# Kernel tuning notes

Hardware: AMD Instinct MI355X
Metric: run time of the kernel (lower is better)

Reference implementation:

```python
import jax, jax.numpy as jnp
import numpy as np

B = 8192
N_IN = 16 * 12 * 64  # 12288
H0, H1, H2 = 256, 32, 32
OUTPUT_SCALE = 300.0
WDL_SCALE = 200.0


def setup_inputs() -> dict:
    key = jax.random.key(0)
    ks = jax.random.split(key, 12)
    # In real NNUE these are ~30-hot binary vectors; math is identical for dense rand.
    white_features = (jax.random.uniform(ks[0], (B, N_IN)) < 0.0025).astype(jnp.float32)
    black_features = (jax.random.uniform(ks[1], (B, N_IN)) < 0.0025).astype(jnp.float32)
    side = jax.random.randint(ks[2], (B,), 0, 2).astype(bool)
    ft_std = np.sqrt(2.0 / (22 + H1))
    ft_w = jax.random.normal(ks[3], (H0, N_IN)) * ft_std
    ft_b = jnp.zeros((H0,))
    def xavier(k, fan_out, fan_in):
        std = np.sqrt(2.0 / (fan_in + fan_out))
        return jax.random.normal(k, (fan_out, fan_in)) * std
    l1_w = xavier(ks[4], H1, 2 * H0)
    l1_b = jnp.zeros((H1,))
    l2_w = xavier(ks[5], H2, H1)
    l2_b = jnp.zeros((H2,))
    l3_w = xavier(ks[6], 1, H2)
    l3_b = jnp.zeros((1,))
    return {"white_features": white_features, "black_features": black_features,
            "side": side, "ft_w": ft_w, "ft_b": ft_b, "l1_w": l1_w, "l1_b": l1_b,
            "l2_w": l2_w, "l2_b": l2_b, "l3_w": l3_w, "l3_b": l3_b}


def reference(white_features, black_features, side, ft_w, ft_b,
              l1_w, l1_b, l2_w, l2_b, l3_w, l3_b):
    w = white_features @ ft_w.T + ft_b  # [B, H0]
    b = black_features @ ft_w.T + ft_b  # [B, H0]
    s = side[:, None]  # [B, 1] bool
    # side-to-move first: white -> [w, b], black -> [b, w]
    acc = jnp.where(s, jnp.concatenate([w, b], axis=1),
                    jnp.concatenate([b, w], axis=1))  # [B, 2*H0]
    o0 = jnp.clip(acc, 0.0, 1.0)
    o1 = jnp.clip(o0 @ l1_w.T + l1_b, 0.0, 1.0)
    o2 = jnp.clip(o1 @ l2_w.T + l2_b, 0.0, 1.0)
    o3 = (o2 @ l3_w.T + l3_b) * OUTPUT_SCALE  # [B, 1]
    return jax.nn.sigmoid(o3 / WDL_SCALE)
```

## Files before the change

### kernel.cpp

```cpp
#include <hip/hip_runtime.h>
#include <math.h>


#define NIN   12288
#define NF4   3072
#define FPT   12
#define H0    256
#define MAXF  192

__device__ __forceinline__ unsigned char mask4(uint4 u) {
    return (unsigned char)((u.x ? 1u : 0u) | (u.y ? 2u : 0u) |
                           (u.z ? 4u : 0u) | (u.w ? 8u : 0u));
}
__device__ __forceinline__ float bflo(unsigned u) { return __uint_as_float(u << 16); }
__device__ __forceinline__ float bfhi(unsigned u) { return __uint_as_float(u & 0xFFFF0000u); }

__global__ __launch_bounds__(256) void transpose_ftw_bf16(const float* __restrict__ src,
                                                          unsigned short* __restrict__ dst) {
    __shared__ float tile[32][33];
    const int jb = blockIdx.x * 32;
    const int hb = blockIdx.y * 32;
    const int tx = threadIdx.x;
    const int ty = threadIdx.y;
#pragma unroll
    for (int r = 0; r < 32; r += 8)
        tile[ty + r][tx] = src[(size_t)(hb + ty + r) * NIN + jb + tx];
    __syncthreads();
#pragma unroll
    for (int r = 0; r < 32; r += 8) {
        const unsigned u = __float_as_uint(tile[tx][ty + r]);
        const unsigned short h = (unsigned short)((u + 0x7FFFu + ((u >> 16) & 1u)) >> 16);
        dst[(size_t)(jb + ty + r) * H0 + hb + tx] = h;
    }
}

__global__ __launch_bounds__(256, 4) void scan_kernel(const uint4* __restrict__ white,
                                                      const uint4* __restrict__ black,
                                                      unsigned char* __restrict__ wbm,
                                                      unsigned char* __restrict__ bbm,
                                                      int total)
{
    const int i0 = blockIdx.x * 2048 + threadIdx.x;
    if (i0 + 7 * 256 < total) {
        uint4 w[8], b[8];
#pragma unroll
        for (int k = 0; k < 8; ++k) w[k] = white[i0 + k * 256];
#pragma unroll
        for (int k = 0; k < 8; ++k) b[k] = black[i0 + k * 256];
#pragma unroll
        for (int k = 0; k < 8; ++k) wbm[i0 + k * 256] = mask4(w[k]);
#pragma unroll
        for (int k = 0; k < 8; ++k) bbm[i0 + k * 256] = mask4(b[k]);
    } else {
#pragma unroll
        for (int k = 0; k < 8; ++k) {
            const int i = i0 + k * 256;
            if (i < total) { wbm[i] = mask4(white[i]); bbm[i] = mask4(black[i]); }
        }
    }
}

__global__ __launch_bounds__(256) void gather_kernel(
    const int* __restrict__ side,
    const unsigned* __restrict__ tab,
    const float* __restrict__ ft_b,
    const float* __restrict__ l1_w,
    const float* __restrict__ l1_b,
    const float* __restrict__ l2_w,
    const float* __restrict__ l2_b,
    const float* __restrict__ l3_w,
    const float* __restrict__ l3_b,
    const unsigned char* __restrict__ wbm,
    const unsigned char* __restrict__ bbm,
    float* __restrict__ out)
{
    __shared__ int w_list[MAXF];
    __shared__ int b_list[MAXF];
    __shared__ int w_cnt, b_cnt;
    __shared__ float sh_o0[512] __attribute__((aligned(16)));
    __shared__ float sh_o1[32];
    __shared__ float sh_o2[32];

    const int s   = blockIdx.x;
    const int tid = threadIdx.x;

    if (tid == 0) { w_cnt = 0; b_cnt = 0; }
    __syncthreads();

    const unsigned* wrow = (const unsigned*)(wbm + (size_t)s * NF4);
    const unsigned* brow = (const unsigned*)(bbm + (size_t)s * NF4);
#pragma unroll
    for (int q = 0; q < 3; ++q) {
        const int d = q * 256 + tid;
        unsigned v = wrow[d];
        while (v) {
            const int bpos = __ffs(v) - 1;
            const int j = ((d * 4 + (bpos >> 3)) << 2) + (bpos & 7);
            const int p = atomicAdd(&w_cnt, 1);
            if (p < MAXF) w_list[p] = j;
            v &= v - 1;
        }
        unsigned vb = brow[d];
        while (vb) {
            const int bpos = __ffs(vb) - 1;
            const int j = ((d * 4 + (bpos >> 3)) << 2) + (bpos & 7);
            const int p = atomicAdd(&b_cnt, 1);
            if (p < MAXF) b_list[p] = j;
            vb &= vb - 1;
        }
    }
    __syncthreads();

    const int wn = min(w_cnt, MAXF);
    const int bn = min(b_cnt, MAXF);

    const int  h       = tid & 127;
    const bool isWhite = (tid < 128);
    const int* lst     = isWhite ? w_list : b_list;
    const int  n       = isWhite ? wn : bn;
    const unsigned* colp = tab + h;

    float accx = ft_b[2 * h];
    float accy = ft_b[2 * h + 1];
    {
        int k = 0;
        for (; k + 8 <= n; k += 8) {
            const unsigned u0 = colp[(size_t)lst[k]     * 128];
            const unsigned u1 = colp[(size_t)lst[k + 1] * 128];
            const unsigned u2 = colp[(size_t)lst[k + 2] * 128];
            const unsigned u3 = colp[(size_t)lst[k + 3] * 128];
            const unsigned u4 = colp[(size_t)lst[k + 4] * 128];
            const unsigned u5 = colp[(size_t)lst[k + 5] * 128];
            const unsigned u6 = colp[(size_t)lst[k + 6] * 128];
            const unsigned u7 = colp[(size_t)lst[k + 7] * 128];
            accx += ((bflo(u0) + bflo(u1)) + (bflo(u2) + bflo(u3))) +
                    ((bflo(u4) + bflo(u5)) + (bflo(u6) + bflo(u7)));
            accy += ((bfhi(u0) + bfhi(u1)) + (bfhi(u2) + bfhi(u3))) +
                    ((bfhi(u4) + bfhi(u5)) + (bfhi(u6) + bfhi(u7)));
        }
        for (; k < n; ++k) {
            const unsigned u = colp[(size_t)lst[k] * 128];
            accx += bflo(u);
            accy += bfhi(u);
        }
    }
    const float cx = fminf(fmaxf(accx, 0.f), 1.f);
    const float cy = fminf(fmaxf(accy, 0.f), 1.f);
    const bool sd = (side[s] != 0);
    const int base = (isWhite == sd) ? 0 : 256;
    sh_o0[base + 2 * h]     = cx;
    sh_o0[base + 2 * h + 1] = cy;
    __syncthreads();

    {
        const int o = tid >> 3;
        const int p = tid & 7;
        const float4* wp = (const float4*)(l1_w + (o * 512 + p * 64));
        const float4* xp = (const float4*)(sh_o0 + p * 64);
        float sum = 0.f;
#pragma unroll
        for (int i = 0; i < 16; ++i) {
            const int v = (2 * p + i) & 15;
            float4 w4 = wp[v];
            float4 x4 = xp[v];
            sum += w4.x * x4.x + w4.y * x4.y + w4.z * x4.z + w4.w * x4.w;
        }
        sum += __shfl_down(sum, 4, 8);
        sum += __shfl_down(sum, 2, 8);
        sum += __shfl_down(sum, 1, 8);
        if (p == 0) sh_o1[o] = fminf(fmaxf(sum + l1_b[o], 0.f), 1.f);
    }
    __syncthreads();

    if (tid < 32) {
        float sum = 0.f;
#pragma unroll
        for (int k = 0; k < 32; ++k) sum += l2_w[tid * 32 + k] * sh_o1[k];
        sh_o2[tid] = fminf(fmaxf(sum + l2_b[tid], 0.f), 1.f);
    }
    __syncthreads();

    if (tid < 32) {
        float p = l3_w[tid] * sh_o2[tid];
        p += __shfl_down(p, 16, 32);
        p += __shfl_down(p, 8, 32);
        p += __shfl_down(p, 4, 32);
        p += __shfl_down(p, 2, 32);
        p += __shfl_down(p, 1, 32);
        if (tid == 0) {
            const float o3 = (p + l3_b[0]) * 300.0f;
            out[s] = 1.0f / (1.0f + expf(-o3 / 200.0f));
        }
    }
}

__global__ __launch_bounds__(256) void nnue_kernel(
    const float* __restrict__ white, const float* __restrict__ black,
    const int* __restrict__ side, const float* __restrict__ ftw,
    const float* __restrict__ ft_b, const float* __restrict__ l1_w,
    const float* __restrict__ l1_b, const float* __restrict__ l2_w,
    const float* __restrict__ l2_b, const float* __restrict__ l3_w,
    const float* __restrict__ l3_b, float* __restrict__ out)
{
    __shared__ int w_list[MAXF];
    __shared__ int b_list[MAXF];
    __shared__ int w_cnt, b_cnt;
    __shared__ float sh_o0[512] __attribute__((aligned(16)));
    __shared__ float sh_o1[32];
    __shared__ float sh_o2[32];
    const int s = blockIdx.x, tid = threadIdx.x;
    if (tid == 0) { w_cnt = 0; b_cnt = 0; }
    __syncthreads();
    const uint4* wrow = (const uint4*)(white + (size_t)s * NIN);
    const uint4* brow = (const uint4*)(black + (size_t)s * NIN);
#pragma unroll
    for (int i = 0; i < FPT; ++i) {
        const int v = i * 256 + tid;
        uint4 u = wrow[v];
        if (u.x | u.y | u.z | u.w) {
            if (u.x) { int p = atomicAdd(&w_cnt, 1); if (p < MAXF) w_list[p] = v * 4 + 0; }
            if (u.y) { int p = atomicAdd(&w_cnt, 1); if (p < MAXF) w_list[p] = v * 4 + 1; }
            if (u.z) { int p = atomicAdd(&w_cnt, 1); if (p < MAXF) w_list[p] = v * 4 + 2; }
            if (u.w) { int p = atomicAdd(&w_cnt, 1); if (p < MAXF) w_list[p] = v * 4 + 3; }
        }
        uint4 b = brow[v];
        if (b.x | b.y | b.z | b.w) {
            if (b.x) { int p = atomicAdd(&b_cnt, 1); if (p < MAXF) b_list[p] = v * 4 + 0; }
            if (b.y) { int p = atomicAdd(&b_cnt, 1); if (p < MAXF) b_list[p] = v * 4 + 1; }
            if (b.z) { int p = atomicAdd(&b_cnt, 1); if (p < MAXF) b_list[p] = v * 4 + 2; }
            if (b.w) { int p = atomicAdd(&b_cnt, 1); if (p < MAXF) b_list[p] = v * 4 + 3; }
        }
    }
    __syncthreads();
    const int wn = min(w_cnt, MAXF), bn = min(b_cnt, MAXF);
    const float bias = ft_b[tid];
    float wacc = bias, bacc = bias;
    for (int k = 0; k < wn; ++k) wacc += ftw[(size_t)tid * NIN + w_list[k]];
    for (int k = 0; k < bn; ++k) bacc += ftw[(size_t)tid * NIN + b_list[k]];
    const float ow = fminf(fmaxf(wacc, 0.f), 1.f);
    const float ob = fminf(fmaxf(bacc, 0.f), 1.f);
    const bool sd = (side[s] != 0);
    sh_o0[tid] = sd ? ow : ob;
    sh_o0[256 + tid] = sd ? ob : ow;
    __syncthreads();
    {
        const int o = tid >> 3, p = tid & 7;
        const float4* wp = (const float4*)(l1_w + (o * 512 + p * 64));
        const float4* xp = (const float4*)(sh_o0 + p * 64);
        float sum = 0.f;
#pragma unroll
        for (int i = 0; i < 16; ++i) {
            const int v = (2 * p + i) & 15;
            float4 w4 = wp[v]; float4 x4 = xp[v];
            sum += w4.x * x4.x + w4.y * x4.y + w4.z * x4.z + w4.w * x4.w;
        }
        sum += __shfl_down(sum, 4, 8);
        sum += __shfl_down(sum, 2, 8);
        sum += __shfl_down(sum, 1, 8);
        if (p == 0) sh_o1[o] = fminf(fmaxf(sum + l1_b[o], 0.f), 1.f);
    }
    __syncthreads();
    if (tid < 32) {
        float sum = 0.f;
#pragma unroll
        for (int k = 0; k < 32; ++k) sum += l2_w[tid * 32 + k] * sh_o1[k];
        sh_o2[tid] = fminf(fmaxf(sum + l2_b[tid], 0.f), 1.f);
    }
    __syncthreads();
    if (tid < 32) {
        float p = l3_w[tid] * sh_o2[tid];
        p += __shfl_down(p, 16, 32);
        p += __shfl_down(p, 8, 32);
        p += __shfl_down(p, 4, 32);
        p += __shfl_down(p, 2, 32);
        p += __shfl_down(p, 1, 32);
        if (tid == 0) {
            const float o3 = (p + l3_b[0]) * 300.0f;
            out[s] = 1.0f / (1.0f + expf(-o3 / 200.0f));
        }
    }
}

extern "C" void kernel_launch(void* const* d_in, const int* in_sizes, int n_in,
                              void* d_out, int out_size, void* d_ws, size_t ws_size,
                              hipStream_t stream) {
    const float* white = (const float*)d_in[0];
    const float* black = (const float*)d_in[1];
    const int*   side  = (const int*)d_in[2];
    const float* ft_w  = (const float*)d_in[3];
    const float* ft_b  = (const float*)d_in[4];
    const float* l1_w  = (const float*)d_in[5];
    const float* l1_b  = (const float*)d_in[6];
    const float* l2_w  = (const float*)d_in[7];
    const float* l2_b  = (const float*)d_in[8];
    const float* l3_w  = (const float*)d_in[9];
    const float* l3_b  = (const float*)d_in[10];
    float*       out   = (float*)d_out;

    const int B = in_sizes[2];
    const size_t t_bytes  = (size_t)NIN * H0 * 2;
    const size_t bm_bytes = (size_t)B * NF4;
    const size_t need     = t_bytes + 2 * bm_bytes;

    if (ws_size >= need) {
        unsigned short* ftw_t = (unsigned short*)d_ws;
        unsigned char*  wbm   = (unsigned char*)d_ws + t_bytes;
        unsigned char*  bbm   = wbm + bm_bytes;
        const int total = B * NF4;

        hipLaunchKernelGGL(transpose_ftw_bf16, dim3(NIN / 32, H0 / 32), dim3(32, 8), 0, stream,
                           ft_w, ftw_t);
        hipLaunchKernelGGL(scan_kernel, dim3((total + 2047) / 2048), dim3(256), 0, stream,
                           (const uint4*)white, (const uint4*)black, wbm, bbm, total);
        hipLaunchKernelGGL(gather_kernel, dim3(B), dim3(256), 0, stream,
                           side, (const unsigned*)ftw_t, ft_b, l1_w, l1_b, l2_w, l2_b,
                           l3_w, l3_b, wbm, bbm, out);
    } else {
        hipLaunchKernelGGL(nnue_kernel, dim3(B), dim3(256), 0, stream,
                           white, black, side, ft_w, ft_b, l1_w, l1_b, l2_w, l2_b,
                           l3_w, l3_b, out);
    }
}
```

Measured before the change: 883.8 us.

## Fuse dense feature scan into gather kernel, dropping bitmask intermediate pass

Removes the separate scan kernel that compressed the dense float feature rows into 4-bit masks in workspace. The gather kernel now reads the dense white/black rows directly, batching four uint4 loads per side before building the active-feature lists with shared atomics. This saves a kernel launch and the write and re-read of the bitmask buffers. In exchange, each block streams 96KB of dense input itself, and the per-block scan may expose memory latency that the wide, high-occupancy scan kernel used to hide.

```diff
diff --git a/kernel.cpp b/kernel.cpp
--- a/kernel.cpp
+++ b/kernel.cpp
@@ -4,14 +4,9 @@
 
 #define NIN   12288
 #define NF4   3072
-#define FPT   12
 #define H0    256
 #define MAXF  192
 
-__device__ __forceinline__ unsigned char mask4(uint4 u) {
-    return (unsigned char)((u.x ? 1u : 0u) | (u.y ? 2u : 0u) |
-                           (u.z ? 4u : 0u) | (u.w ? 8u : 0u));
-}
 __device__ __forceinline__ float bflo(unsigned u) { return __uint_as_float(u << 16); }
 __device__ __forceinline__ float bfhi(unsigned u) { return __uint_as_float(u & 0xFFFF0000u); }
 
@@ -34,33 +29,9 @@
     }
 }
 
-__global__ __launch_bounds__(256, 4) void scan_kernel(const uint4* __restrict__ white,
-                                                      const uint4* __restrict__ black,
-                                                      unsigned char* __restrict__ wbm,
-                                                      unsigned char* __restrict__ bbm,
-                                                      int total)
-{
-    const int i0 = blockIdx.x * 2048 + threadIdx.x;
-    if (i0 + 7 * 256 < total) {
-        uint4 w[8], b[8];
-#pragma unroll
-        for (int k = 0; k < 8; ++k) w[k] = white[i0 + k * 256];
-#pragma unroll
-        for (int k = 0; k < 8; ++k) b[k] = black[i0 + k * 256];
-#pragma unroll
-        for (int k = 0; k < 8; ++k) wbm[i0 + k * 256] = mask4(w[k]);
-#pragma unroll
-        for (int k = 0; k < 8; ++k) bbm[i0 + k * 256] = mask4(b[k]);
-    } else {
-#pragma unroll
-        for (int k = 0; k < 8; ++k) {
-            const int i = i0 + k * 256;
-            if (i < total) { wbm[i] = mask4(white[i]); bbm[i] = mask4(black[i]); }
-        }
-    }
-}
-
-__global__ __launch_bounds__(256) void gather_kernel(
+__global__ __launch_bounds__(256) void nnue_mono(
+    const float* __restrict__ white,
+    const float* __restrict__ black,
     const int* __restrict__ side,
     const unsigned* __restrict__ tab,
     const float* __restrict__ ft_b,
@@ -70,8 +41,6 @@
     const float* __restrict__ l2_b,
     const float* __restrict__ l3_w,
     const float* __restrict__ l3_b,
-    const unsigned char* __restrict__ wbm,
-    const unsigned char* __restrict__ bbm,
     float* __restrict__ out)
 {
     __shared__ int w_list[MAXF];
@@ -87,26 +56,32 @@
     if (tid == 0) { w_cnt = 0; b_cnt = 0; }
     __syncthreads();
 
-    const unsigned* wrow = (const unsigned*)(wbm + (size_t)s * NF4);
-    const unsigned* brow = (const unsigned*)(bbm + (size_t)s * NF4);
-#pragma unroll
-    for (int q = 0; q < 3; ++q) {
-        const int d = q * 256 + tid;
-        unsigned v = wrow[d];
-        while (v) {
-            const int bpos = __ffs(v) - 1;
-            const int j = ((d * 4 + (bpos >> 3)) << 2) + (bpos & 7);
-            const int p = atomicAdd(&w_cnt, 1);
-            if (p < MAXF) w_list[p] = j;
-            v &= v - 1;
-        }
-        unsigned vb = brow[d];
-        while (vb) {
-            const int bpos = __ffs(vb) - 1;
-            const int j = ((d * 4 + (bpos >> 3)) << 2) + (bpos & 7);
-            const int p = atomicAdd(&b_cnt, 1);
-            if (p < MAXF) b_list[p] = j;
-            vb &= vb - 1;
+    const uint4* wrow = (const uint4*)(white + (size_t)s * NIN);
+    const uint4* brow = (const uint4*)(black + (size_t)s * NIN);
+#pragma unroll
+    for (int i = 0; i < 3; ++i) {
+        uint4 w4[4], b4[4];
+#pragma unroll
+        for (int k = 0; k < 4; ++k) w4[k] = wrow[(i * 4 + k) * 256 + tid];
+#pragma unroll
+        for (int k = 0; k < 4; ++k) b4[k] = brow[(i * 4 + k) * 256 + tid];
+#pragma unroll
+        for (int k = 0; k < 4; ++k) {
+            const int v = (i * 4 + k) * 256 + tid;
+            const uint4 u = w4[k];
+            if (u.x | u.y | u.z | u.w) {
+                if (u.x) { int p = atomicAdd(&w_cnt, 1); if (p < MAXF) w_list[p] = v * 4 + 0; }
+                if (u.y) { int p = atomicAdd(&w_cnt, 1); if (p < MAXF) w_list[p] = v * 4 + 1; }
+                if (u.z) { int p = atomicAdd(&w_cnt, 1); if (p < MAXF) w_list[p] = v * 4 + 2; }
+                if (u.w) { int p = atomicAdd(&w_cnt, 1); if (p < MAXF) w_list[p] = v * 4 + 3; }
+            }
+            const uint4 b = b4[k];
+            if (b.x | b.y | b.z | b.w) {
+                if (b.x) { int p = atomicAdd(&b_cnt, 1); if (p < MAXF) b_list[p] = v * 4 + 0; }
+                if (b.y) { int p = atomicAdd(&b_cnt, 1); if (p < MAXF) b_list[p] = v * 4 + 1; }
+                if (b.z) { int p = atomicAdd(&b_cnt, 1); if (p < MAXF) b_list[p] = v * 4 + 2; }
+                if (b.w) { int p = atomicAdd(&b_cnt, 1); if (p < MAXF) b_list[p] = v * 4 + 3; }
+            }
         }
     }
     __syncthreads();
@@ -214,7 +189,7 @@
     const uint4* wrow = (const uint4*)(white + (size_t)s * NIN);
     const uint4* brow = (const uint4*)(black + (size_t)s * NIN);
 #pragma unroll
-    for (int i = 0; i < FPT; ++i) {
+    for (int i = 0; i < 12; ++i) {
         const int v = i * 256 + tid;
         uint4 u = wrow[v];
         if (u.x | u.y | u.z | u.w) {
@@ -298,23 +273,15 @@
     float*       out   = (float*)d_out;
 
     const int B = in_sizes[2];
-    const size_t t_bytes  = (size_t)NIN * H0 * 2;
-    const size_t bm_bytes = (size_t)B * NF4;
-    const size_t need     = t_bytes + 2 * bm_bytes;
-
-    if (ws_size >= need) {
+    const size_t t_bytes = (size_t)NIN * H0 * 2;
+
+    if (ws_size >= t_bytes) {
         unsigned short* ftw_t = (unsigned short*)d_ws;
-        unsigned char*  wbm   = (unsigned char*)d_ws + t_bytes;
-        unsigned char*  bbm   = wbm + bm_bytes;
-        const int total = B * NF4;
-
         hipLaunchKernelGGL(transpose_ftw_bf16, dim3(NIN / 32, H0 / 32), dim3(32, 8), 0, stream,
                            ft_w, ftw_t);
-        hipLaunchKernelGGL(scan_kernel, dim3((total + 2047) / 2048), dim3(256), 0, stream,
-                           (const uint4*)white, (const uint4*)black, wbm, bbm, total);
-        hipLaunchKernelGGL(gather_kernel, dim3(B), dim3(256), 0, stream,
-                           side, (const unsigned*)ftw_t, ft_b, l1_w, l1_b, l2_w, l2_b,
-                           l3_w, l3_b, wbm, bbm, out);
+        hipLaunchKernelGGL(nnue_mono, dim3(B), dim3(256), 0, stream,
+                           white, black, side, (const unsigned*)ftw_t, ft_b,
+                           l1_w, l1_b, l2_w, l2_b, l3_w, l3_b, out);
     } else {
         hipLaunchKernelGGL(nnue_kernel, dim3(B), dim3(256), 0, stream,
                            white, black, side, ft_w, ft_b, l1_w, l1_b, l2_w, l2_b,
```

New measurement: 795.2 us. 1.11x faster.
